# Kernel optimization log

Hardware: AMD Instinct MI355X
Metric: run time of the kernel (lower is better)

## Reference

```python
import jax, jax.numpy as jnp
import numpy as np

N_NODES = 50000
N_EDGES = 800000
EMB = 128
HID = [128, 128]
OUT = 64
CE = 8  # stand-in for CROSS_ENTROPY_INDEXES: first 8 output columns get sigmoid


def _linear_params(key, d_in, d_out):
    k1, k2 = jax.random.split(key)
    s = 1.0 / np.sqrt(d_in)
    w = jax.random.uniform(k1, (d_in, d_out), minval=-s, maxval=s, dtype=jnp.float32)
    b = jax.random.uniform(k2, (d_out,), minval=-s, maxval=s, dtype=jnp.float32)
    return w, b


def setup_inputs() -> dict:
    key = jax.random.key(0)
    ks = jax.random.split(key, 16)
    z = jax.random.normal(ks[0], (N_NODES, EMB), dtype=jnp.float32)
    edge_index = jax.random.randint(ks[1], (2, N_EDGES), 0, N_NODES, dtype=jnp.int64)
    # SAGEConv params: neighbor weight (with bias) + root weight
    w1_n, b1 = _linear_params(ks[2], EMB, HID[0])
    w1_r, _ = _linear_params(ks[3], EMB, HID[0])
    w2_n, b2 = _linear_params(ks[4], HID[0], HID[1])
    w2_r, _ = _linear_params(ks[5], HID[0], HID[1])
    wf_n, bf = _linear_params(ks[6], HID[1], OUT)
    wf_r, _ = _linear_params(ks[7], HID[1], OUT)
    # initial residual linears: emb -> hid[1], emb -> out
    w_res1, b_res1 = _linear_params(ks[8], EMB, HID[1])
    w_res2, b_res2 = _linear_params(ks[9], EMB, OUT)
    return dict(z=z, edge_index=edge_index,
                w1_n=w1_n, w1_r=w1_r, b1=b1,
                w2_n=w2_n, w2_r=w2_r, b2=b2,
                wf_n=wf_n, wf_r=wf_r, bf=bf,
                w_res1=w_res1, b_res1=b_res1,
                w_res2=w_res2, b_res2=b_res2)


def _sage(x, src, dst, w_n, w_r, b, n_nodes):
    # mean-aggregate neighbor features at target nodes, then affine combine with root
    msg = x[src]                                        # [E, d]
    agg = jax.ops.segment_sum(msg, dst, num_segments=n_nodes)
    deg = jax.ops.segment_sum(jnp.ones_like(dst, dtype=x.dtype), dst, num_segments=n_nodes)
    mean = agg / jnp.maximum(deg, 1.0)[:, None]
    return mean @ w_n + x @ w_r + b


def reference(z, edge_index, w1_n, w1_r, b1, w2_n, w2_r, b2, wf_n, wf_r, bf,
              w_res1, b_res1, w_res2, b_res2):
    n = z.shape[0]
    src, dst = edge_index[0], edge_index[1]
    h = jax.nn.relu(_sage(z, src, dst, w1_n, w1_r, b1, n))
    # mid layer (dropout is identity in eval) + initial residual
    h = jax.nn.relu(_sage(h, src, dst, w2_n, w2_r, b2, n))
    h = h + (z @ w_res1 + b_res1)
    # final conv + final residual
    h = _sage(h, src, dst, wf_n, wf_r, bf, n)
    h = h + (z @ w_res2 + b_res2)
    # sigmoid on cross-entropy columns
    h = h.at[:, :CE].set(jax.nn.sigmoid(h[:, :CE]))
    return h
```

## Files before the change

kernel.cpp:

```cpp
#include <hip/hip_runtime.h>
#include <hip/hip_bf16.h>
#include <math.h>

#define NN 50000
#define NE 800000
#define NB 391
#define EPB 6250

typedef short bf16x8 __attribute__((ext_vector_type(8)));
typedef float f32x4 __attribute__((ext_vector_type(4)));
typedef unsigned short us4 __attribute__((ext_vector_type(4)));
typedef unsigned short us8 __attribute__((ext_vector_type(8)));
typedef unsigned int u32x4 __attribute__((ext_vector_type(4)));

__device__ __forceinline__ float bf2f(unsigned short u) {
  union { unsigned int i; float f; } x; x.i = ((unsigned int)u) << 16; return x.f;
}
__device__ __forceinline__ unsigned short f2bf(float f) {
  union { float f; unsigned int i; } x; x.f = f;
  unsigned int i = x.i;
  unsigned int r = i + 0x7FFF + ((i >> 16) & 1);
  return (unsigned short)(r >> 16);
}
__device__ __forceinline__ us4 pack4(f32x4 v) {
  us4 o; o[0] = f2bf(v[0]); o[1] = f2bf(v[1]); o[2] = f2bf(v[2]); o[3] = f2bf(v[3]);
  return o;
}

__global__ __launch_bounds__(256) void bhist_kernel(const int* __restrict__ dstn,
                                                    int* __restrict__ bhist) {
  __shared__ int h[NB];
  for (int i = threadIdx.x; i < NB; i += 256) h[i] = 0;
  __syncthreads();
  int e0 = blockIdx.x * EPB;
  for (int i = threadIdx.x; i < EPB; i += 256)
    atomicAdd(&h[dstn[e0 + i] >> 7], 1);
  __syncthreads();
  for (int i = threadIdx.x; i < NB; i += 256)
    if (h[i]) atomicAdd(&bhist[i], h[i]);
}

__global__ __launch_bounds__(512) void bscan_kernel(const int* __restrict__ bhist,
                                                    int* __restrict__ bucket_off,
                                                    int* __restrict__ gcur) {
  __shared__ int s[512];
  int t = threadIdx.x;
  int v = (t < NB) ? bhist[t] : 0;
  s[t] = v; __syncthreads();
  for (int off = 1; off < 512; off <<= 1) {
    int x = (t >= off) ? s[t - off] : 0;
    __syncthreads();
    s[t] += x;
    __syncthreads();
  }
  if (t < NB) { bucket_off[t] = s[t] - v; gcur[t] = 0; }
  if (t == NB - 1) bucket_off[NB] = s[t];
}

__global__ __launch_bounds__(256) void bscat_kernel(const int* __restrict__ srcn,
                                                    const int* __restrict__ dstn,
                                                    const int* __restrict__ bucket_off,
                                                    int* __restrict__ gcur,
                                                    unsigned long long* __restrict__ ebuf) {
  __shared__ int hist[NB];
  __shared__ int base[NB];
  for (int i = threadIdx.x; i < NB; i += 256) hist[i] = 0;
  __syncthreads();
  int e0 = blockIdx.x * EPB;
  for (int i = threadIdx.x; i < EPB; i += 256)
    atomicAdd(&hist[dstn[e0 + i] >> 7], 1);
  __syncthreads();
  for (int i = threadIdx.x; i < NB; i += 256) {
    int c = hist[i];
    base[i] = c ? (bucket_off[i] + atomicAdd(&gcur[i], c)) : 0;
  }
  __syncthreads();
  for (int i = threadIdx.x; i < EPB; i += 256) {
    int s = srcn[e0 + i], d = dstn[e0 + i];
    int b = d >> 7;
    int pos = atomicSub(&hist[b], 1) - 1;
    ebuf[(size_t)base[b] + pos] = ((unsigned long long)(unsigned)d << 32) | (unsigned)s;
  }
}

__global__ __launch_bounds__(256) void bfill_kernel(const unsigned long long* __restrict__ ebuf,
                                                    const int* __restrict__ bucket_off,
                                                    int* __restrict__ rowoff,
                                                    int* __restrict__ csr) {
  int b = blockIdx.x;
  int bo = bucket_off[b], cnt = bucket_off[b + 1] - bo;
  __shared__ int ndeg[128], noff[128];
  int t = threadIdx.x;
  if (t < 128) ndeg[t] = 0;
  __syncthreads();
  for (int i = t; i < cnt; i += 256)
    atomicAdd(&ndeg[(int)(ebuf[bo + i] >> 32) & 127], 1);
  __syncthreads();
  if (t < 128) noff[t] = ndeg[t];
  __syncthreads();
  for (int off = 1; off < 128; off <<= 1) {
    int x = 0;
    if (t < 128 && t >= off) x = noff[t - off];
    __syncthreads();
    if (t < 128 && t >= off) noff[t] += x;
    __syncthreads();
  }
  if (t < 128) {
    int ex = noff[t] - ndeg[t];
    noff[t] = ex;
    int node = b * 128 + t;
    if (node < NN) rowoff[node] = bo + ex;
  }
  if (b == NB - 1 && t == 0) rowoff[NN] = NE;
  __syncthreads();
  for (int i = t; i < cnt; i += 256) {
    unsigned long long e = ebuf[bo + i];
    int dl = (int)(e >> 32) & 127;
    int pos = atomicSub(&ndeg[dl], 1) - 1;
    csr[bo + noff[dl] + pos] = (int)(unsigned)e;
  }
}

__global__ void prep_kernel(const float* __restrict__ w1n, const float* __restrict__ w1r,
                            const float* __restrict__ w2n, const float* __restrict__ w2r,
                            const float* __restrict__ wfn, const float* __restrict__ wfr,
                            const float* __restrict__ wr1, const float* __restrict__ wr2,
                            unsigned short* __restrict__ Bp1, unsigned short* __restrict__ Bp2,
                            unsigned short* __restrict__ Bp3) {
  int g = blockIdx.x * 256 + threadIdx.x;
  unsigned short* D; int NT, fi;
  int which;
  if      (g < 10240) { fi = g;         D = Bp1; NT = 20; which = 1; }
  else if (g < 14336) { fi = g - 10240; D = Bp2; NT = 8;  which = 2; }
  else if (g < 16384) { fi = g - 14336; D = Bp3; NT = 4;  which = 3; }
  else return;
  int lane = fi & 63, t = fi >> 6;
  int nt = t % NT, k0i = t / NT;
  int m = lane & 15, q = lane >> 4;
  int kb = k0i * 32 + q * 8;
  int n = nt * 16 + m;
  int hi = (kb >= 128);
  int k0_ = kb - (hi ? 128 : 0);
  const float* W = nullptr; int Nseg = 128; int nn = n;
  if (which == 1) {
    if (n < 128)      { W = hi ? w1r : w1n; nn = n; Nseg = 128; }
    else if (n < 256) { W = hi ? wr1 : nullptr; nn = n - 128; Nseg = 128; }
    else              { W = hi ? wr2 : nullptr; nn = n - 256; Nseg = 64; }
  } else if (which == 2) { W = hi ? w2r : w2n; Nseg = 128; }
  else                   { W = hi ? wfr : wfn; Nseg = 64; }
  unsigned short o[8];
#pragma unroll
  for (int j = 0; j < 8; j++)
    o[j] = W ? f2bf(W[(size_t)(k0_ + j) * Nseg + nn]) : (unsigned short)0;
  *(us8*)(D + (size_t)fi * 8) = *(const us8*)o;
}

__global__ void convz_kernel(const float* __restrict__ z, unsigned short* __restrict__ A1) {
  int i = blockIdx.x * 256 + threadIdx.x;
  if (i >= NN * 128 / 4) return;
  int i4 = i * 4;
  int row = i4 >> 7, c = i4 & 127;
  float4 v = *(const float4*)(z + i4);
  us4 o = { f2bf(v.x), f2bf(v.y), f2bf(v.z), f2bf(v.w) };
  *(us4*)(A1 + (size_t)row * 256 + 128 + c) = o;
}

__global__ __launch_bounds__(256) void agg_kernel(const unsigned short* __restrict__ feat, int fstride,
                                                  unsigned short* __restrict__ outm, int ostride,
                                                  const int* __restrict__ rowoff,
                                                  const int* __restrict__ csr) {
  int wave = threadIdx.x >> 6, lane = threadIdx.x & 63;
  int node = blockIdx.x * 4 + wave;
  if (node >= NN) return;
  int beg = rowoff[node], end = rowoff[node + 1];
  int g = lane >> 4;
  int c = (lane & 15) << 3;
  float a[8];
#pragma unroll
  for (int i = 0; i < 8; i++) a[i] = 0.f;
  int j = beg + g;
  for (; j + 12 < end; j += 16) {
    int s0 = csr[j];
    int s1 = csr[j + 4];
    int s2 = csr[j + 8];
    int s3 = csr[j + 12];
    u32x4 v0 = *(const u32x4*)(feat + (size_t)s0 * fstride + c);
    u32x4 v1 = *(const u32x4*)(feat + (size_t)s1 * fstride + c);
    u32x4 v2 = *(const u32x4*)(feat + (size_t)s2 * fstride + c);
    u32x4 v3 = *(const u32x4*)(feat + (size_t)s3 * fstride + c);
#pragma unroll
    for (int i = 0; i < 4; i++) {
      a[2*i]   += bf2f((unsigned short)(v0[i] & 0xffff)) + bf2f((unsigned short)(v1[i] & 0xffff))
                + bf2f((unsigned short)(v2[i] & 0xffff)) + bf2f((unsigned short)(v3[i] & 0xffff));
      a[2*i+1] += bf2f((unsigned short)(v0[i] >> 16)) + bf2f((unsigned short)(v1[i] >> 16))
                + bf2f((unsigned short)(v2[i] >> 16)) + bf2f((unsigned short)(v3[i] >> 16));
    }
  }
  for (; j < end; j += 4) {
    int s0 = csr[j];
    u32x4 v0 = *(const u32x4*)(feat + (size_t)s0 * fstride + c);
#pragma unroll
    for (int i = 0; i < 4; i++) {
      a[2*i]   += bf2f((unsigned short)(v0[i] & 0xffff));
      a[2*i+1] += bf2f((unsigned short)(v0[i] >> 16));
    }
  }
#pragma unroll
  for (int i = 0; i < 8; i++) {
    a[i] += __shfl_xor(a[i], 16, 64);
    a[i] += __shfl_xor(a[i], 32, 64);
  }
  if (g == 0) {
    float inv = 1.f / fmaxf((float)(end - beg), 1.f);
    unsigned int o[4];
#pragma unroll
    for (int i = 0; i < 4; i++)
      o[i] = ((unsigned int)f2bf(a[2*i+1] * inv) << 16) | f2bf(a[2*i] * inv);
    *(u32x4*)(outm + (size_t)node * ostride + c) = *(const u32x4*)o;
  }
}

__global__ __launch_bounds__(256) void gemm1_kernel(
    const unsigned short* __restrict__ A,
    const unsigned short* __restrict__ Bp,
    const float* __restrict__ b1, const float* __restrict__ br1, const float* __restrict__ br2,
    unsigned short* __restrict__ h1out,
    unsigned short* __restrict__ res1, unsigned short* __restrict__ res2)
{
  const int NT = 20, TILES = 5;
  __shared__ unsigned short Bs[TILES * 8 * 512];
  int tid = threadIdx.x;
  int wave = tid >> 6, lane = tid & 63;
  int ybase = blockIdx.x * TILES;
#pragma unroll
  for (int i = tid; i < TILES * 64 * 8; i += 256) {
    int k0i = i / (TILES * 64), r = i % (TILES * 64);
    *(us8*)(Bs + (size_t)k0i * TILES * 512 + (size_t)r * 8) =
        *(const us8*)(Bp + ((size_t)k0i * NT + ybase) * 512 + (size_t)r * 8);
  }
  int row0 = blockIdx.y * 64 + wave * 16;
  int m = lane & 15, q = lane >> 4;
  const unsigned short* arow = A + (size_t)(row0 + m) * 256 + q * 8;
  bf16x8 af[8];
#pragma unroll
  for (int k0i = 0; k0i < 8; ++k0i) af[k0i] = *(const bf16x8*)(arow + k0i * 32);
  __syncthreads();
  f32x4 acc[TILES];
#pragma unroll
  for (int i = 0; i < TILES; i++) acc[i] = (f32x4){0.f, 0.f, 0.f, 0.f};
#pragma unroll
  for (int k0i = 0; k0i < 8; ++k0i) {
    const unsigned short* bk = Bs + (size_t)k0i * TILES * 512 + lane * 8;
#pragma unroll
    for (int s = 0; s < TILES; ++s) {
      bf16x8 bfr = *(const bf16x8*)(bk + s * 512);
      acc[s] = __builtin_amdgcn_mfma_f32_16x16x32_bf16(bfr, af[k0i], acc[s], 0, 0, 0);
    }
  }
  int row = row0 + m;
  if (row >= NN) return;
  int cb = q * 4;
#pragma unroll
  for (int s = 0; s < TILES; ++s) {
    int nt = ybase + s;
    f32x4 v = acc[s];
    if (nt < 8) {
      int col = nt * 16 + cb;
      float4 bb = *(const float4*)(b1 + col);
      v[0] = fmaxf(v[0] + bb.x, 0.f); v[1] = fmaxf(v[1] + bb.y, 0.f);
      v[2] = fmaxf(v[2] + bb.z, 0.f); v[3] = fmaxf(v[3] + bb.w, 0.f);
      *(us4*)(h1out + (size_t)row * 256 + col) = pack4(v);
    } else if (nt < 16) {
      int col = (nt - 8) * 16 + cb;
      float4 bb = *(const float4*)(br1 + col);
      v[0] += bb.x; v[1] += bb.y; v[2] += bb.z; v[3] += bb.w;
      *(us4*)(res1 + (size_t)row * 128 + col) = pack4(v);
    } else {
      int col = (nt - 16) * 16 + cb;
      float4 bb = *(const float4*)(br2 + col);
      v[0] += bb.x; v[1] += bb.y; v[2] += bb.z; v[3] += bb.w;
      *(us4*)(res2 + (size_t)row * 64 + col) = pack4(v);
    }
  }
}

template <int NTT>
__global__ __launch_bounds__(256) void gemm23_kernel(
    const unsigned short* __restrict__ A,
    const unsigned short* __restrict__ Bp,
    const float* __restrict__ bias,
    const unsigned short* __restrict__ res, int res_stride,
    unsigned short* __restrict__ out_bf,
    float* __restrict__ out_f, int of_stride,
    int relu, int sig8)
{
  const int TILES = 4;
  __shared__ unsigned short Bs[TILES * 8 * 512];
  int tid = threadIdx.x;
  int wave = tid >> 6, lane = tid & 63;
  int ybase = blockIdx.x * TILES;
#pragma unroll
  for (int i = tid; i < TILES * 64 * 8; i += 256) {
    int k0i = i / (TILES * 64), r = i % (TILES * 64);
    *(us8*)(Bs + (size_t)k0i * TILES * 512 + (size_t)r * 8) =
        *(const us8*)(Bp + ((size_t)k0i * NTT + ybase) * 512 + (size_t)r * 8);
  }
  int row0 = blockIdx.y * 64 + wave * 16;
  int m = lane & 15, q = lane >> 4;
  const unsigned short* arow = A + (size_t)(row0 + m) * 256 + q * 8;
  bf16x8 af[8];
#pragma unroll
  for (int k0i = 0; k0i < 8; ++k0i) af[k0i] = *(const bf16x8*)(arow + k0i * 32);
  __syncthreads();
  f32x4 acc[TILES];
#pragma unroll
  for (int i = 0; i < TILES; i++) acc[i] = (f32x4){0.f, 0.f, 0.f, 0.f};
#pragma unroll
  for (int k0i = 0; k0i < 8; ++k0i) {
    const unsigned short* bk = Bs + (size_t)k0i * TILES * 512 + lane * 8;
#pragma unroll
    for (int s = 0; s < TILES; ++s) {
      bf16x8 bfr = *(const bf16x8*)(bk + s * 512);
      acc[s] = __builtin_amdgcn_mfma_f32_16x16x32_bf16(bfr, af[k0i], acc[s], 0, 0, 0);
    }
  }
  int row = row0 + m;
  if (row >= NN) return;
  int cb = q * 4;
#pragma unroll
  for (int s = 0; s < TILES; ++s) {
    int col = (ybase + s) * 16 + cb;
    f32x4 v = acc[s];
    float4 bb = *(const float4*)(bias + col);
    v[0] += bb.x; v[1] += bb.y; v[2] += bb.z; v[3] += bb.w;
    if (relu) {
#pragma unroll
      for (int r = 0; r < 4; r++) v[r] = fmaxf(v[r], 0.f);
    }
    if (res) {
      us4 rv = *(const us4*)(res + (size_t)row * res_stride + col);
#pragma unroll
      for (int r = 0; r < 4; r++) v[r] += bf2f(rv[r]);
    }
    if (sig8 && col < 8) {
#pragma unroll
      for (int r = 0; r < 4; r++) v[r] = 1.f / (1.f + __expf(-v[r]));
    }
    if (out_bf) *(us4*)(out_bf + (size_t)row * 256 + col) = pack4(v);
    if (out_f) {
      float4 o = { v[0], v[1], v[2], v[3] };
      *(float4*)(out_f + (size_t)row * of_stride + col) = o;
    }
  }
}

extern "C" void kernel_launch(void* const* d_in, const int* in_sizes, int n_in,
                              void* d_out, int out_size, void* d_ws, size_t ws_size,
                              hipStream_t stream) {
  const float* z   = (const float*)d_in[0];
  const int*   edge = (const int*)d_in[1];
  const int*   srcn = edge;
  const int*   dstn = edge + NE;
  const float* w1n = (const float*)d_in[2];
  const float* w1r = (const float*)d_in[3];
  const float* b1  = (const float*)d_in[4];
  const float* w2n = (const float*)d_in[5];
  const float* w2r = (const float*)d_in[6];
  const float* b2  = (const float*)d_in[7];
  const float* wfn = (const float*)d_in[8];
  const float* wfr = (const float*)d_in[9];
  const float* bfb = (const float*)d_in[10];
  const float* wr1 = (const float*)d_in[11];
  const float* br1 = (const float*)d_in[12];
  const float* wr2 = (const float*)d_in[13];
  const float* br2 = (const float*)d_in[14];
  float* out = (float*)d_out;

  char* p = (char*)d_ws;
  auto alloc = [&](size_t bytes) { char* r = p; p += (bytes + 255) & ~255ull; return r; };
  int* rowoff = (int*)alloc((size_t)(NN + 1) * 4);
  int* bhist  = (int*)alloc((size_t)NB * 4);
  int* bucket_off = (int*)alloc((size_t)(NB + 1) * 4);
  int* gcur   = (int*)alloc((size_t)NB * 4);
  int* csr    = (int*)alloc((size_t)NE * 4);
  unsigned short* A1 = (unsigned short*)alloc((size_t)NN * 256 * 2);
  unsigned short* A2 = (unsigned short*)alloc((size_t)NN * 256 * 2);
  unsigned short* res1 = (unsigned short*)alloc((size_t)NN * 128 * 2);
  unsigned short* res2 = (unsigned short*)alloc((size_t)NN * 64 * 2);
  unsigned short* Bp1 = (unsigned short*)alloc(10240 * 8 * 2);
  unsigned short* Bp2 = (unsigned short*)alloc(4096 * 8 * 2);
  unsigned short* Bp3 = (unsigned short*)alloc(2048 * 8 * 2);
  unsigned short* A3 = A1;
  unsigned long long* ebuf = (unsigned long long*)res1;

  hipMemsetAsync(bhist, 0, (size_t)NB * 4, stream);
  bhist_kernel<<<128, 256, 0, stream>>>(dstn, bhist);
  bscan_kernel<<<1, 512, 0, stream>>>(bhist, bucket_off, gcur);
  bscat_kernel<<<128, 256, 0, stream>>>(srcn, dstn, bucket_off, gcur, ebuf);
  bfill_kernel<<<NB, 256, 0, stream>>>(ebuf, bucket_off, rowoff, csr);

  prep_kernel<<<64, 256, 0, stream>>>(w1n, w1r, w2n, w2r, wfn, wfr, wr1, wr2, Bp1, Bp2, Bp3);
  convz_kernel<<<(NN * 128 / 4 + 255) / 256, 256, 0, stream>>>(z, A1);

  const int gy = (NN + 63) / 64;
  const int agg_blocks = (NN + 3) / 4;

  agg_kernel<<<agg_blocks, 256, 0, stream>>>(A1 + 128, 256, A1, 256, rowoff, csr);
  gemm1_kernel<<<dim3(4, gy), 256, 0, stream>>>(A1, Bp1, b1, br1, br2, A2 + 128, res1, res2);

  agg_kernel<<<agg_blocks, 256, 0, stream>>>(A2 + 128, 256, A2, 256, rowoff, csr);
  gemm23_kernel<8><<<dim3(2, gy), 256, 0, stream>>>(A2, Bp2, b2, res1, 128,
      A3 + 128, nullptr, 0, 1, 0);

  agg_kernel<<<agg_blocks, 256, 0, stream>>>(A3 + 128, 256, A3, 256, rowoff, csr);
  gemm23_kernel<4><<<dim3(1, gy), 256, 0, stream>>>(A3, Bp3, bfb, res2, 64,
      nullptr, out, 64, 0, 1);
}
```

Baseline: 297.6 us.

## Fuse setup kernels, branchless agg tail, and two row tiles per GEMM wave

Merges the bf16 conversion of z, the weight prepacking and the bucket histogram into one launch to cut launch overhead. The aggregation loop now has no scalar tail loop: out-of-range edges are clamped to the last edge and weighted by zero, so every iteration issues four gathers. gemm1 and gemm2 now have each wave compute two 16-row tiles that share the same B fragments, which halves B staging per row and halves the grid. A-fragment loads are moved ahead of the B staging to overlap them. The costs are higher register pressure in the GEMMs, some redundant gathers for low-degree nodes, and padded-row loads past NN in the last block.

```diff
diff --git a/kernel.cpp b/kernel.cpp
--- a/kernel.cpp
+++ b/kernel.cpp
@@ -25,19 +25,6 @@
 __device__ __forceinline__ us4 pack4(f32x4 v) {
   us4 o; o[0] = f2bf(v[0]); o[1] = f2bf(v[1]); o[2] = f2bf(v[2]); o[3] = f2bf(v[3]);
   return o;
-}
-
-__global__ __launch_bounds__(256) void bhist_kernel(const int* __restrict__ dstn,
-                                                    int* __restrict__ bhist) {
-  __shared__ int h[NB];
-  for (int i = threadIdx.x; i < NB; i += 256) h[i] = 0;
-  __syncthreads();
-  int e0 = blockIdx.x * EPB;
-  for (int i = threadIdx.x; i < EPB; i += 256)
-    atomicAdd(&h[dstn[e0 + i] >> 7], 1);
-  __syncthreads();
-  for (int i = threadIdx.x; i < NB; i += 256)
-    if (h[i]) atomicAdd(&bhist[i], h[i]);
 }
 
 __global__ __launch_bounds__(512) void bscan_kernel(const int* __restrict__ bhist,
@@ -121,48 +108,62 @@
   }
 }
 
-__global__ void prep_kernel(const float* __restrict__ w1n, const float* __restrict__ w1r,
-                            const float* __restrict__ w2n, const float* __restrict__ w2r,
-                            const float* __restrict__ wfn, const float* __restrict__ wfr,
-                            const float* __restrict__ wr1, const float* __restrict__ wr2,
-                            unsigned short* __restrict__ Bp1, unsigned short* __restrict__ Bp2,
-                            unsigned short* __restrict__ Bp3) {
-  int g = blockIdx.x * 256 + threadIdx.x;
-  unsigned short* D; int NT, fi;
-  int which;
-  if      (g < 10240) { fi = g;         D = Bp1; NT = 20; which = 1; }
-  else if (g < 14336) { fi = g - 10240; D = Bp2; NT = 8;  which = 2; }
-  else if (g < 16384) { fi = g - 14336; D = Bp3; NT = 4;  which = 3; }
-  else return;
-  int lane = fi & 63, t = fi >> 6;
-  int nt = t % NT, k0i = t / NT;
-  int m = lane & 15, q = lane >> 4;
-  int kb = k0i * 32 + q * 8;
-  int n = nt * 16 + m;
-  int hi = (kb >= 128);
-  int k0_ = kb - (hi ? 128 : 0);
-  const float* W = nullptr; int Nseg = 128; int nn = n;
-  if (which == 1) {
-    if (n < 128)      { W = hi ? w1r : w1n; nn = n; Nseg = 128; }
-    else if (n < 256) { W = hi ? wr1 : nullptr; nn = n - 128; Nseg = 128; }
-    else              { W = hi ? wr2 : nullptr; nn = n - 256; Nseg = 64; }
-  } else if (which == 2) { W = hi ? w2r : w2n; Nseg = 128; }
-  else                   { W = hi ? wfr : wfn; Nseg = 64; }
-  unsigned short o[8];
-#pragma unroll
-  for (int j = 0; j < 8; j++)
-    o[j] = W ? f2bf(W[(size_t)(k0_ + j) * Nseg + nn]) : (unsigned short)0;
-  *(us8*)(D + (size_t)fi * 8) = *(const us8*)o;
-}
-
-__global__ void convz_kernel(const float* __restrict__ z, unsigned short* __restrict__ A1) {
-  int i = blockIdx.x * 256 + threadIdx.x;
-  if (i >= NN * 128 / 4) return;
-  int i4 = i * 4;
-  int row = i4 >> 7, c = i4 & 127;
-  float4 v = *(const float4*)(z + i4);
-  us4 o = { f2bf(v.x), f2bf(v.y), f2bf(v.z), f2bf(v.w) };
-  *(us4*)(A1 + (size_t)row * 256 + 128 + c) = o;
+__global__ __launch_bounds__(256) void setup_kernel(
+    const float* __restrict__ z, unsigned short* __restrict__ A1,
+    const float* __restrict__ w1n, const float* __restrict__ w1r,
+    const float* __restrict__ w2n, const float* __restrict__ w2r,
+    const float* __restrict__ wfn, const float* __restrict__ wfr,
+    const float* __restrict__ wr1, const float* __restrict__ wr2,
+    unsigned short* __restrict__ Bp1, unsigned short* __restrict__ Bp2,
+    unsigned short* __restrict__ Bp3,
+    const int* __restrict__ dstn, int* __restrict__ bhist) {
+  __shared__ int h[NB];
+  int b = blockIdx.x;
+  if (b < 6250) {
+    int i = b * 256 + threadIdx.x;
+    if (i >= NN * 128 / 4) return;
+    int i4 = i * 4;
+    int row = i4 >> 7, c = i4 & 127;
+    float4 v = *(const float4*)(z + i4);
+    us4 o = { f2bf(v.x), f2bf(v.y), f2bf(v.z), f2bf(v.w) };
+    *(us4*)(A1 + (size_t)row * 256 + 128 + c) = o;
+  } else if (b < 6314) {
+    int g = (b - 6250) * 256 + threadIdx.x;
+    unsigned short* D; int NT, fi;
+    int which;
+    if      (g < 10240) { fi = g;         D = Bp1; NT = 20; which = 1; }
+    else if (g < 14336) { fi = g - 10240; D = Bp2; NT = 8;  which = 2; }
+    else if (g < 16384) { fi = g - 14336; D = Bp3; NT = 4;  which = 3; }
+    else return;
+    int lane = fi & 63, t = fi >> 6;
+    int nt = t % NT, k0i = t / NT;
+    int m = lane & 15, q = lane >> 4;
+    int kb = k0i * 32 + q * 8;
+    int n = nt * 16 + m;
+    int hi = (kb >= 128);
+    int k0_ = kb - (hi ? 128 : 0);
+    const float* W = nullptr; int Nseg = 128; int nn = n;
+    if (which == 1) {
+      if (n < 128)      { W = hi ? w1r : w1n; nn = n; Nseg = 128; }
+      else if (n < 256) { W = hi ? wr1 : nullptr; nn = n - 128; Nseg = 128; }
+      else              { W = hi ? wr2 : nullptr; nn = n - 256; Nseg = 64; }
+    } else if (which == 2) { W = hi ? w2r : w2n; Nseg = 128; }
+    else                   { W = hi ? wfr : wfn; Nseg = 64; }
+    unsigned short o[8];
+#pragma unroll
+    for (int j = 0; j < 8; j++)
+      o[j] = W ? f2bf(W[(size_t)(k0_ + j) * Nseg + nn]) : (unsigned short)0;
+    *(us8*)(D + (size_t)fi * 8) = *(const us8*)o;
+  } else {
+    for (int i = threadIdx.x; i < NB; i += 256) h[i] = 0;
+    __syncthreads();
+    int e0 = (b - 6314) * EPB;
+    for (int i = threadIdx.x; i < EPB; i += 256)
+      atomicAdd(&h[dstn[e0 + i] >> 7], 1);
+    __syncthreads();
+    for (int i = threadIdx.x; i < NB; i += 256)
+      if (h[i]) atomicAdd(&bhist[i], h[i]);
+  }
 }
 
 __global__ __launch_bounds__(256) void agg_kernel(const unsigned short* __restrict__ feat, int fstride,
@@ -178,31 +179,31 @@
   float a[8];
 #pragma unroll
   for (int i = 0; i < 8; i++) a[i] = 0.f;
-  int j = beg + g;
-  for (; j + 12 < end; j += 16) {
-    int s0 = csr[j];
-    int s1 = csr[j + 4];
-    int s2 = csr[j + 8];
-    int s3 = csr[j + 12];
+  int e1 = end - 1;
+  for (int j = beg + g; j < end; j += 16) {
+    int j1 = (j + 4 < e1) ? j + 4 : e1;
+    int j2 = (j + 8 < e1) ? j + 8 : e1;
+    int j3 = (j + 12 < e1) ? j + 12 : e1;
+    int s0 = csr[j], s1 = csr[j1], s2 = csr[j2], s3 = csr[j3];
+    float w1 = (j + 4 < end) ? 1.f : 0.f;
+    float w2 = (j + 8 < end) ? 1.f : 0.f;
+    float w3 = (j + 12 < end) ? 1.f : 0.f;
     u32x4 v0 = *(const u32x4*)(feat + (size_t)s0 * fstride + c);
     u32x4 v1 = *(const u32x4*)(feat + (size_t)s1 * fstride + c);
     u32x4 v2 = *(const u32x4*)(feat + (size_t)s2 * fstride + c);
     u32x4 v3 = *(const u32x4*)(feat + (size_t)s3 * fstride + c);
 #pragma unroll
     for (int i = 0; i < 4; i++) {
-      a[2*i]   += bf2f((unsigned short)(v0[i] & 0xffff)) + bf2f((unsigned short)(v1[i] & 0xffff))
-                + bf2f((unsigned short)(v2[i] & 0xffff)) + bf2f((unsigned short)(v3[i] & 0xffff));
-      a[2*i+1] += bf2f((unsigned short)(v0[i] >> 16)) + bf2f((unsigned short)(v1[i] >> 16))
-                + bf2f((unsigned short)(v2[i] >> 16)) + bf2f((unsigned short)(v3[i] >> 16));
-    }
-  }
-  for (; j < end; j += 4) {
-    int s0 = csr[j];
-    u32x4 v0 = *(const u32x4*)(feat + (size_t)s0 * fstride + c);
-#pragma unroll
-    for (int i = 0; i < 4; i++) {
-      a[2*i]   += bf2f((unsigned short)(v0[i] & 0xffff));
-      a[2*i+1] += bf2f((unsigned short)(v0[i] >> 16));
+      float l0 = bf2f((unsigned short)(v0[i] & 0xffff));
+      float h0 = bf2f((unsigned short)(v0[i] >> 16));
+      l0 = fmaf(w1, bf2f((unsigned short)(v1[i] & 0xffff)), l0);
+      h0 = fmaf(w1, bf2f((unsigned short)(v1[i] >> 16)), h0);
+      l0 = fmaf(w2, bf2f((unsigned short)(v2[i] & 0xffff)), l0);
+      h0 = fmaf(w2, bf2f((unsigned short)(v2[i] >> 16)), h0);
+      l0 = fmaf(w3, bf2f((unsigned short)(v3[i] & 0xffff)), l0);
+      h0 = fmaf(w3, bf2f((unsigned short)(v3[i] >> 16)), h0);
+      a[2*i] += l0;
+      a[2*i+1] += h0;
     }
   }
 #pragma unroll
@@ -232,59 +233,69 @@
   int tid = threadIdx.x;
   int wave = tid >> 6, lane = tid & 63;
   int ybase = blockIdx.x * TILES;
+  int row0 = blockIdx.y * 128 + wave * 16;
+  int m = lane & 15, q = lane >> 4;
+  const unsigned short* arow0 = A + (size_t)(row0 + m) * 256 + q * 8;
+  const unsigned short* arow1 = arow0 + 64 * 256;
+  bf16x8 af0[8], af1[8];
+#pragma unroll
+  for (int k0i = 0; k0i < 8; ++k0i) {
+    af0[k0i] = *(const bf16x8*)(arow0 + k0i * 32);
+    af1[k0i] = *(const bf16x8*)(arow1 + k0i * 32);
+  }
 #pragma unroll
   for (int i = tid; i < TILES * 64 * 8; i += 256) {
     int k0i = i / (TILES * 64), r = i % (TILES * 64);
     *(us8*)(Bs + (size_t)k0i * TILES * 512 + (size_t)r * 8) =
         *(const us8*)(Bp + ((size_t)k0i * NT + ybase) * 512 + (size_t)r * 8);
   }
-  int row0 = blockIdx.y * 64 + wave * 16;
-  int m = lane & 15, q = lane >> 4;
-  const unsigned short* arow = A + (size_t)(row0 + m) * 256 + q * 8;
-  bf16x8 af[8];
-#pragma unroll
-  for (int k0i = 0; k0i < 8; ++k0i) af[k0i] = *(const bf16x8*)(arow + k0i * 32);
-  __syncthreads();
-  f32x4 acc[TILES];
-#pragma unroll
-  for (int i = 0; i < TILES; i++) acc[i] = (f32x4){0.f, 0.f, 0.f, 0.f};
+  __syncthreads();
+  f32x4 acc[2][TILES];
+#pragma unroll
+  for (int h = 0; h < 2; h++)
+#pragma unroll
+    for (int i = 0; i < TILES; i++) acc[h][i] = (f32x4){0.f, 0.f, 0.f, 0.f};
 #pragma unroll
   for (int k0i = 0; k0i < 8; ++k0i) {
     const unsigned short* bk = Bs + (size_t)k0i * TILES * 512 + lane * 8;
 #pragma unroll
     for (int s = 0; s < TILES; ++s) {
       bf16x8 bfr = *(const bf16x8*)(bk + s * 512);
-      acc[s] = __builtin_amdgcn_mfma_f32_16x16x32_bf16(bfr, af[k0i], acc[s], 0, 0, 0);
+      acc[0][s] = __builtin_amdgcn_mfma_f32_16x16x32_bf16(bfr, af0[k0i], acc[0][s], 0, 0, 0);
+      acc[1][s] = __builtin_amdgcn_mfma_f32_16x16x32_bf16(bfr, af1[k0i], acc[1][s], 0, 0, 0);
     }
   }
-  int row = row0 + m;
-  if (row >= NN) return;
   int cb = q * 4;
 #pragma unroll
-  for (int s = 0; s < TILES; ++s) {
-    int nt = ybase + s;
-    f32x4 v = acc[s];
-    if (nt < 8) {
-      int col = nt * 16 + cb;
-      float4 bb = *(const float4*)(b1 + col);
-      v[0] = fmaxf(v[0] + bb.x, 0.f); v[1] = fmaxf(v[1] + bb.y, 0.f);
-      v[2] = fmaxf(v[2] + bb.z, 0.f); v[3] = fmaxf(v[3] + bb.w, 0.f);
-      *(us4*)(h1out + (size_t)row * 256 + col) = pack4(v);
-    } else if (nt < 16) {
-      int col = (nt - 8) * 16 + cb;
-      float4 bb = *(const float4*)(br1 + col);
-      v[0] += bb.x; v[1] += bb.y; v[2] += bb.z; v[3] += bb.w;
-      *(us4*)(res1 + (size_t)row * 128 + col) = pack4(v);
-    } else {
-      int col = (nt - 16) * 16 + cb;
-      float4 bb = *(const float4*)(br2 + col);
-      v[0] += bb.x; v[1] += bb.y; v[2] += bb.z; v[3] += bb.w;
-      *(us4*)(res2 + (size_t)row * 64 + col) = pack4(v);
+  for (int h = 0; h < 2; h++) {
+    int row = row0 + h * 64 + m;
+    if (row >= NN) continue;
+#pragma unroll
+    for (int s = 0; s < TILES; ++s) {
+      int nt = ybase + s;
+      f32x4 v = acc[h][s];
+      if (nt < 8) {
+        int col = nt * 16 + cb;
+        float4 bb = *(const float4*)(b1 + col);
+        v[0] = fmaxf(v[0] + bb.x, 0.f); v[1] = fmaxf(v[1] + bb.y, 0.f);
+        v[2] = fmaxf(v[2] + bb.z, 0.f); v[3] = fmaxf(v[3] + bb.w, 0.f);
+        *(us4*)(h1out + (size_t)row * 256 + col) = pack4(v);
+      } else if (nt < 16) {
+        int col = (nt - 8) * 16 + cb;
+        float4 bb = *(const float4*)(br1 + col);
+        v[0] += bb.x; v[1] += bb.y; v[2] += bb.z; v[3] += bb.w;
+        *(us4*)(res1 + (size_t)row * 128 + col) = pack4(v);
+      } else {
+        int col = (nt - 16) * 16 + cb;
+        float4 bb = *(const float4*)(br2 + col);
+        v[0] += bb.x; v[1] += bb.y; v[2] += bb.z; v[3] += bb.w;
+        *(us4*)(res2 + (size_t)row * 64 + col) = pack4(v);
+      }
     }
   }
 }
 
-template <int NTT>
+template <int NTT, int RPW>
 __global__ __launch_bounds__(256) void gemm23_kernel(
     const unsigned short* __restrict__ A,
     const unsigned short* __restrict__ Bp,
@@ -299,57 +310,67 @@
   int tid = threadIdx.x;
   int wave = tid >> 6, lane = tid & 63;
   int ybase = blockIdx.x * TILES;
+  int row0 = blockIdx.y * (64 * RPW) + wave * 16;
+  int m = lane & 15, q = lane >> 4;
+  bf16x8 af[RPW][8];
+#pragma unroll
+  for (int h = 0; h < RPW; h++) {
+    const unsigned short* arow = A + (size_t)(row0 + h * 64 + m) * 256 + q * 8;
+#pragma unroll
+    for (int k0i = 0; k0i < 8; ++k0i) af[h][k0i] = *(const bf16x8*)(arow + k0i * 32);
+  }
 #pragma unroll
   for (int i = tid; i < TILES * 64 * 8; i += 256) {
     int k0i = i / (TILES * 64), r = i % (TILES * 64);
     *(us8*)(Bs + (size_t)k0i * TILES * 512 + (size_t)r * 8) =
         *(const us8*)(Bp + ((size_t)k0i * NTT + ybase) * 512 + (size_t)r * 8);
   }
-  int row0 = blockIdx.y * 64 + wave * 16;
-  int m = lane & 15, q = lane >> 4;
-  const unsigned short* arow = A + (size_t)(row0 + m) * 256 + q * 8;
-  bf16x8 af[8];
-#pragma unroll
-  for (int k0i = 0; k0i < 8; ++k0i) af[k0i] = *(const bf16x8*)(arow + k0i * 32);
-  __syncthreads();
-  f32x4 acc[TILES];
-#pragma unroll
-  for (int i = 0; i < TILES; i++) acc[i] = (f32x4){0.f, 0.f, 0.f, 0.f};
+  __syncthreads();
+  f32x4 acc[RPW][TILES];
+#pragma unroll
+  for (int h = 0; h < RPW; h++)
+#pragma unroll
+    for (int i = 0; i < TILES; i++) acc[h][i] = (f32x4){0.f, 0.f, 0.f, 0.f};
 #pragma unroll
   for (int k0i = 0; k0i < 8; ++k0i) {
     const unsigned short* bk = Bs + (size_t)k0i * TILES * 512 + lane * 8;
 #pragma unroll
     for (int s = 0; s < TILES; ++s) {
       bf16x8 bfr = *(const bf16x8*)(bk + s * 512);
-      acc[s] = __builtin_amdgcn_mfma_f32_16x16x32_bf16(bfr, af[k0i], acc[s], 0, 0, 0);
+#pragma unroll
+      for (int h = 0; h < RPW; h++)
+        acc[h][s] = __builtin_amdgcn_mfma_f32_16x16x32_bf16(bfr, af[h][k0i], acc[h][s], 0, 0, 0);
     }
   }
-  int row = row0 + m;
-  if (row >= NN) return;
   int cb = q * 4;
 #pragma unroll
-  for (int s = 0; s < TILES; ++s) {
-    int col = (ybase + s) * 16 + cb;
-    f32x4 v = acc[s];
-    float4 bb = *(const float4*)(bias + col);
-    v[0] += bb.x; v[1] += bb.y; v[2] += bb.z; v[3] += bb.w;
-    if (relu) {
-#pragma unroll
-      for (int r = 0; r < 4; r++) v[r] = fmaxf(v[r], 0.f);
-    }
-    if (res) {
-      us4 rv = *(const us4*)(res + (size_t)row * res_stride + col);
-#pragma unroll
-      for (int r = 0; r < 4; r++) v[r] += bf2f(rv[r]);
-    }
-    if (sig8 && col < 8) {
-#pragma unroll
-      for (int r = 0; r < 4; r++) v[r] = 1.f / (1.f + __expf(-v[r]));
-    }
-    if (out_bf) *(us4*)(out_bf + (size_t)row * 256 + col) = pack4(v);
-    if (out_f) {
-      float4 o = { v[0], v[1], v[2], v[3] };
-      *(float4*)(out_f + (size_t)row * of_stride + col) = o;
+  for (int h = 0; h < RPW; h++) {
+    int row = row0 + h * 64 + m;
+    if (row >= NN) continue;
+#pragma unroll
+    for (int s = 0; s < TILES; ++s) {
+      int col = (ybase + s) * 16 + cb;
+      f32x4 v = acc[h][s];
+      float4 bb = *(const float4*)(bias + col);
+      v[0] += bb.x; v[1] += bb.y; v[2] += bb.z; v[3] += bb.w;
+      if (relu) {
+#pragma unroll
+        for (int r = 0; r < 4; r++) v[r] = fmaxf(v[r], 0.f);
+      }
+      if (res) {
+        us4 rv = *(const us4*)(res + (size_t)row * res_stride + col);
+#pragma unroll
+        for (int r = 0; r < 4; r++) v[r] += bf2f(rv[r]);
+      }
+      if (sig8 && col < 8) {
+#pragma unroll
+        for (int r = 0; r < 4; r++) v[r] = 1.f / (1.f + __expf(-v[r]));
+      }
+      if (out_bf) *(us4*)(out_bf + (size_t)row * 256 + col) = pack4(v);
+      if (out_f) {
+        float4 o = { v[0], v[1], v[2], v[3] };
+        *(float4*)(out_f + (size_t)row * of_stride + col) = o;
+      }
     }
   }
 }
@@ -394,25 +415,24 @@
   unsigned long long* ebuf = (unsigned long long*)res1;
 
   hipMemsetAsync(bhist, 0, (size_t)NB * 4, stream);
-  bhist_kernel<<<128, 256, 0, stream>>>(dstn, bhist);
+  setup_kernel<<<6442, 256, 0, stream>>>(z, A1, w1n, w1r, w2n, w2r, wfn, wfr, wr1, wr2,
+                                         Bp1, Bp2, Bp3, dstn, bhist);
   bscan_kernel<<<1, 512, 0, stream>>>(bhist, bucket_off, gcur);
   bscat_kernel<<<128, 256, 0, stream>>>(srcn, dstn, bucket_off, gcur, ebuf);
   bfill_kernel<<<NB, 256, 0, stream>>>(ebuf, bucket_off, rowoff, csr);
 
-  prep_kernel<<<64, 256, 0, stream>>>(w1n, w1r, w2n, w2r, wfn, wfr, wr1, wr2, Bp1, Bp2, Bp3);
-  convz_kernel<<<(NN * 128 / 4 + 255) / 256, 256, 0, stream>>>(z, A1);
-
-  const int gy = (NN + 63) / 64;
+  const int gy128 = (NN + 127) / 128;
+  const int gy64  = (NN + 63) / 64;
   const int agg_blocks = (NN + 3) / 4;
 
   agg_kernel<<<agg_blocks, 256, 0, stream>>>(A1 + 128, 256, A1, 256, rowoff, csr);
-  gemm1_kernel<<<dim3(4, gy), 256, 0, stream>>>(A1, Bp1, b1, br1, br2, A2 + 128, res1, res2);
+  gemm1_kernel<<<dim3(4, gy128), 256, 0, stream>>>(A1, Bp1, b1, br1, br2, A2 + 128, res1, res2);
 
   agg_kernel<<<agg_blocks, 256, 0, stream>>>(A2 + 128, 256, A2, 256, rowoff, csr);
-  gemm23_kernel<8><<<dim3(2, gy), 256, 0, stream>>>(A2, Bp2, b2, res1, 128,
+  gemm23_kernel<8, 2><<<dim3(2, gy128), 256, 0, stream>>>(A2, Bp2, b2, res1, 128,
       A3 + 128, nullptr, 0, 1, 0);
 
   agg_kernel<<<agg_blocks, 256, 0, stream>>>(A3 + 128, 256, A3, 256, rowoff, csr);
-  gemm23_kernel<4><<<dim3(1, gy), 256, 0, stream>>>(A3, Bp3, bfb, res2, 64,
+  gemm23_kernel<4, 1><<<dim3(1, gy64), 256, 0, stream>>>(A3, Bp3, bfb, res2, 64,
       nullptr, out, 64, 0, 1);
 }
```

Result: no change. 294.7 us (-1.0%).
